# Kernel tuning notes

Measured on AMD Instinct MI355X. Metric: run time of the kernel, lower is better.

The kernel has to match this reference:

```python
import jax, jax.numpy as jnp
import numpy as np

N, E, D_IN, D_E, H, OUT, L = 16384, 131072, 128, 64, 256, 16, 4
EPS_MSG = 1e-7   # GENConv message epsilon
EPS_SM = 1e-16   # PyG softmax denominator epsilon


def _ln(x, g, b, eps=1e-5):
    mu = x.mean(-1, keepdims=True)
    var = x.var(-1, keepdims=True)
    return (x - mu) * jax.lax.rsqrt(var + eps) * g + b


def _genconv(x, src, dst, e, w1, b1, lng, lnb, w2, b2, t):
    # message: relu(x_j + edge_attr) + eps  -> [E, H]
    msg = jax.nn.relu(x[src] + e) + EPS_MSG
    # learnable-temperature segment softmax over incoming edges, per feature
    m = msg * t
    mx = jax.ops.segment_max(m, dst, num_segments=N)
    mx = jnp.where(jnp.isfinite(mx), mx, 0.0)  # empty segments -> 0
    ex = jnp.exp(m - mx[dst])
    den = jax.ops.segment_sum(ex, dst, num_segments=N)
    alpha = ex / (den[dst] + EPS_SM)
    agg = jax.ops.segment_sum(msg * alpha, dst, num_segments=N)  # [N, H]
    # root residual then 2-layer MLP: Linear -> LayerNorm -> ReLU -> Linear
    out = agg + x
    h = jax.nn.relu(_ln(out @ w1 + b1, lng, lnb))
    return h @ w2 + b2


def setup_inputs() -> dict:
    key = jax.random.key(0)
    ks = jax.random.split(key, 10)
    gl = lambda k, shape, fan: jax.random.normal(k, shape, jnp.float32) / np.sqrt(fan).astype(np.float32)
    return {
        "x": jax.random.normal(ks[0], (N, D_IN), jnp.float32),
        "edge_index": jax.random.randint(ks[1], (2, E), 0, N, dtype=jnp.int32),
        "edge_attr": jax.random.normal(ks[2], (E, D_E), jnp.float32),
        "enc_w": gl(ks[3], (D_IN, H), D_IN), "enc_b": jnp.zeros((H,), jnp.float32),
        "ee_w": gl(ks[4], (D_E, H), D_E), "ee_b": jnp.zeros((H,), jnp.float32),
        "w1": gl(ks[5], (L, H, 2 * H), H), "b1": jnp.zeros((L, 2 * H), jnp.float32),
        "lng": jnp.ones((L, 2 * H), jnp.float32), "lnb": jnp.zeros((L, 2 * H), jnp.float32),
        "w2": gl(ks[6], (L, 2 * H, H), 2 * H), "b2": jnp.zeros((L, H), jnp.float32),
        "t": jnp.ones((L,), jnp.float32),
        "ng": jnp.ones((L, H), jnp.float32), "nb": jnp.zeros((L, H), jnp.float32),
        "lin_w": gl(ks[7], (H, OUT), H), "lin_b": jnp.zeros((OUT,), jnp.float32),
    }


def reference(x, edge_index, edge_attr, enc_w, enc_b, ee_w, ee_b,
              w1, b1, lng, lnb, w2, b2, t, ng, nb, lin_w, lin_b):
    src, dst = edge_index[0], edge_index[1]
    h = x @ enc_w + enc_b                      # node encoder
    e = edge_attr @ ee_w + ee_b                # edge encoder
    # first layer: conv only (per source forward)
    h = _genconv(h, src, dst, e, w1[0], b1[0], lng[0], lnb[0], w2[0], b2[0], t[0])
    # remaining layers: res+ block = x + conv(relu(norm(x)))  (dropout off in eval)
    for i in range(1, L):
        z = jax.nn.relu(_ln(h, ng[i], nb[i]))
        h = h + _genconv(z, src, dst, e, w1[i], b1[i], lng[i], lnb[i], w2[i], b2[i], t[i])
    h = jax.nn.relu(_ln(h, ng[0], nb[0]))      # layers[0].act(layers[0].norm(x))
    return h @ lin_w + lin_b
```

## Files before the change

kernel.cpp:

```cpp
#include <hip/hip_runtime.h>
#include <stdint.h>
#include <math.h>


typedef __bf16 bf16x8 __attribute__((ext_vector_type(8)));
typedef __bf16 bf16x4 __attribute__((ext_vector_type(4)));
typedef float  f32x4  __attribute__((ext_vector_type(4)));

constexpr int NN   = 16384;
constexpr int NE   = 131072;
constexpr int DIN  = 128;
constexpr int DE   = 64;
constexpr int HD   = 256;
constexpr int HD2  = 512;

__device__ __forceinline__ void gl_lds16(const __bf16* g, __bf16* l) {
  __builtin_amdgcn_global_load_lds((const __attribute__((address_space(1))) void*)g,
                                   (__attribute__((address_space(3))) void*)l, 16, 0, 0);
}

__global__ __launch_bounds__(1024) void k_scan(const int* __restrict__ deg,
                                               int* __restrict__ row_start) {
  __shared__ int part[1024];
  const int t = threadIdx.x;
  const int base = t * 16;
  int loc[16];
  int s = 0;
  #pragma unroll
  for (int i = 0; i < 16; i++) { loc[i] = s; s += deg[base + i]; }
  part[t] = s;
  __syncthreads();
  for (int off = 1; off < 1024; off <<= 1) {
    int v = (t >= off) ? part[t - off] : 0;
    __syncthreads();
    part[t] += v;
    __syncthreads();
  }
  const int excl = (t == 0) ? 0 : part[t - 1];
  #pragma unroll
  for (int i = 0; i < 16; i++) row_start[base + i] = excl + loc[i];
}

__global__ void k_scatter(const int* __restrict__ src, const int* __restrict__ dst,
                          const int* __restrict__ row_start, int* __restrict__ cursor,
                          int2* __restrict__ csr_es) {
  int e = blockIdx.x * 256 + threadIdx.x;
  if (e >= NE) return;
  const int d = dst[e];
  const int p = atomicAdd(&cursor[d], 1);
  csr_es[row_start[d] + p] = make_int2(e, src[e]);
}

__global__ __launch_bounds__(256)
void k_sortw(const int* __restrict__ row_start, const int* __restrict__ deg,
             int2* __restrict__ csr_es, int* __restrict__ posmap) {
  const int wv   = threadIdx.x >> 6;
  const int lane = threadIdx.x & 63;
  const int node = blockIdx.x * 4 + wv;
  if (node >= NN) return;
  const int st = __builtin_amdgcn_readfirstlane(row_start[node]);
  const int dg = __builtin_amdgcn_readfirstlane(deg[node]);
  if (dg <= 1) {
    if (dg == 1 && lane == 0) posmap[csr_es[st].x] = st;
    return;
  }
  if (dg <= 64) {
    int2 pr = make_int2(0x7fffffff, 0);
    if (lane < dg) pr = csr_es[st + lane];
    int rank = 0;
    for (int j = 0; j < dg; j++) {
      const int ej = __builtin_amdgcn_readlane(pr.x, j);
      if (lane < dg && ej < pr.x) rank++;
    }
    if (lane < dg) {
      csr_es[st + rank] = pr;
      posmap[pr.x] = st + rank;
    }
  } else if (lane == 0) {
    for (int a = 1; a < dg; a++) {
      int2 k = csr_es[st + a];
      int b = a - 1;
      while (b >= 0 && csr_es[st + b].x > k.x) { csr_es[st + b + 1] = csr_es[st + b]; b--; }
      csr_es[st + b + 1] = k;
    }
    for (int a = 0; a < dg; a++) posmap[csr_es[st + a].x] = st + a;
  }
}

__global__ void k_prep(const float* __restrict__ enc_w, const float* __restrict__ ee_w,
                       const float* __restrict__ w1, const float* __restrict__ w2,
                       const int* __restrict__ dst, int* __restrict__ deg,
                       __bf16* __restrict__ enc_wT, __bf16* __restrict__ ee_wT,
                       __bf16* __restrict__ w1T, __bf16* __restrict__ w2T) {
  int i = blockIdx.x * 256 + threadIdx.x;
  const int S0 = DIN * HD, S1 = DE * HD, S2 = 4 * HD * HD2, S3 = 4 * HD2 * HD;
  if (i < S0) { int k = i / HD, n = i % HD; enc_wT[n * DIN + k] = (__bf16)enc_w[i]; return; }
  i -= S0;
  if (i < S1) { int k = i / HD, n = i % HD; ee_wT[n * DE + k] = (__bf16)ee_w[i]; return; }
  i -= S1;
  if (i < S2) {
    int l = i / (HD * HD2), r = i % (HD * HD2), k = r / HD2, n = r % HD2;
    w1T[(size_t)l * HD * HD2 + (size_t)n * HD + k] = (__bf16)w1[i]; return;
  }
  i -= S2;
  if (i < S3) {
    int l = i / (HD2 * HD), r = i % (HD2 * HD), k = r / HD, n = r % HD;
    w2T[(size_t)l * HD2 * HD + (size_t)n * HD2 + k] = (__bf16)w2[i]; return;
  }
  i -= S3;
  if (i < NE) { atomicAdd(&deg[dst[i]], 1); return; }
}

template <int RES, int OBF, int STATS, int ESCAT, int AF32>
__global__ __launch_bounds__(256, 3)
void k_gemm(const void* __restrict__ Ap, const __bf16* __restrict__ BT,
            const float* __restrict__ bias, const float* __restrict__ R,
            float* __restrict__ Cf, __bf16* __restrict__ Cb,
            const int* __restrict__ posmap, float2* __restrict__ pstats,
            int M, int Nn, int K) {
  __shared__ __attribute__((aligned(16))) char smem[49152];
  float (*sm)[129] = (float(*)[129])smem;
  float* sbias     = (float*)(smem + 16512);
  float2 (*pst4)[32] = (float2(*)[32])(smem + 17024);
  const __bf16* Ab = (const __bf16*)Ap;
  const float*  Af = (const float*)Ap;
  const int tid  = threadIdx.x;
  const int lane = tid & 63;
  const int wave = tid >> 6;
  const int ntn  = Nn >> 7;
  const int bid  = (int)blockIdx.x;
  const int bn   = (bid >> 3) % ntn;
  const int bm   = (bid & 7) + ((bid >> 3) / ntn) * 8;
  const size_t row0 = (size_t)bm * 128, col0 = (size_t)bn * 128;
  const int wr = (wave >> 1) * 64, wc = (wave & 1) * 64;
  const int ks = lane >> 4, fr = lane & 15;

  auto bufA = [&](int i) -> __bf16* { return (__bf16*)(smem + i * 8192); };
  auto bufB = [&](int i) -> __bf16* { return (__bf16*)(smem + 24576 + i * 8192); };

  f32x4 acc[4][4] = {};

  const int arow = tid >> 2;
  const int aksg = (tid & 3) ^ ((arow >> 1) & 3);

  auto stageB = [&](__bf16* lb, int k0) {
    gl_lds16(BT + (col0 + arow) * K + k0 + aksg * 8, &lb[tid * 8]);
    gl_lds16(BT + (col0 + arow + 64) * K + k0 + aksg * 8, &lb[(tid + 256) * 8]);
  };
  auto stageA = [&](__bf16* la, int k0) {
    gl_lds16(Ab + (row0 + arow) * K + k0 + aksg * 8, &la[tid * 8]);
    gl_lds16(Ab + (row0 + arow + 64) * K + k0 + aksg * 8, &la[(tid + 256) * 8]);
  };
  float4 p0, p1, q0, q1;
  auto loadAf = [&](int k0) {
    const float* a0p = &Af[(row0 + arow) * K + k0 + aksg * 8];
    const float* a1p = &Af[(row0 + arow + 64) * K + k0 + aksg * 8];
    p0 = *(const float4*)a0p; p1 = *(const float4*)(a0p + 4);
    q0 = *(const float4*)a1p; q1 = *(const float4*)(a1p + 4);
  };
  auto writeAf = [&](__bf16* la) {
    bf16x8 o0, o1;
    o0[0] = (__bf16)p0.x; o0[1] = (__bf16)p0.y; o0[2] = (__bf16)p0.z; o0[3] = (__bf16)p0.w;
    o0[4] = (__bf16)p1.x; o0[5] = (__bf16)p1.y; o0[6] = (__bf16)p1.z; o0[7] = (__bf16)p1.w;
    o1[0] = (__bf16)q0.x; o1[1] = (__bf16)q0.y; o1[2] = (__bf16)q0.z; o1[3] = (__bf16)q0.w;
    o1[4] = (__bf16)q1.x; o1[5] = (__bf16)q1.y; o1[6] = (__bf16)q1.z; o1[7] = (__bf16)q1.w;
    *(bf16x8*)&la[tid * 8] = o0;
    *(bf16x8*)&la[(tid + 256) * 8] = o1;
  };

  int slA[4], slB[4];
  #pragma unroll
  for (int m = 0; m < 4; m++) {
    const int rm = wr + m * 16 + fr;
    slA[m] = rm * 4 + (ks ^ ((rm >> 1) & 3));
    const int cn = wc + m * 16 + fr;
    slB[m] = cn * 4 + (ks ^ ((cn >> 1) & 3));
  }

  const int nk = K / 32;
  if (AF32) { loadAf(0); stageB(bufB(0), 0); writeAf(bufA(0)); }
  else      { stageA(bufA(0), 0); stageB(bufB(0), 0); }
  if (nk > 1) {
    if (AF32) { loadAf(32); stageB(bufB(1), 32); writeAf(bufA(1)); }
    else      { stageA(bufA(1), 32); stageB(bufB(1), 32); }
  }
  for (int t = 0; t < nk; t++) {
    const int rem = nk - 1 - t;
    const int nb3 = (t + 2) % 3;
    if (rem >= 2) {
      if (AF32) { loadAf((t + 2) * 32); stageB(bufB(nb3), (t + 2) * 32); }
      else      { stageA(bufA(nb3), (t + 2) * 32); stageB(bufB(nb3), (t + 2) * 32); }
    }
    if (AF32) {
      if (rem >= 2)      asm volatile("s_waitcnt vmcnt(8) lgkmcnt(0)" ::: "memory");
      else if (rem == 1) asm volatile("s_waitcnt vmcnt(2) lgkmcnt(0)" ::: "memory");
      else               asm volatile("s_waitcnt vmcnt(0) lgkmcnt(0)" ::: "memory");
    } else {
      if (rem >= 2)      asm volatile("s_waitcnt vmcnt(8)" ::: "memory");
      else if (rem == 1) asm volatile("s_waitcnt vmcnt(4)" ::: "memory");
      else               asm volatile("s_waitcnt vmcnt(0)" ::: "memory");
    }
    __builtin_amdgcn_s_barrier();
    __builtin_amdgcn_sched_barrier(0);
    const __bf16* la = bufA(t % 3);
    const __bf16* lb = bufB(t % 3);
    bf16x8 af[4], bfr[4];
    #pragma unroll
    for (int m = 0; m < 4; m++) af[m]  = *(const bf16x8*)&la[slA[m] * 8];
    #pragma unroll
    for (int n = 0; n < 4; n++) bfr[n] = *(const bf16x8*)&lb[slB[n] * 8];
    #pragma unroll
    for (int m = 0; m < 4; m++)
      #pragma unroll
      for (int n = 0; n < 4; n++)
        acc[m][n] = __builtin_amdgcn_mfma_f32_16x16x32_bf16(af[m], bfr[n], acc[m][n], 0, 0, 0);
    if (AF32 && rem >= 2) writeAf(bufA(nb3));
    __builtin_amdgcn_s_barrier();
  }
  __syncthreads();

  if (tid < 128) sbias[tid] = bias[col0 + tid];
  const int rbase = (wave >> 1) * 16 + ks * 4;
  const int rr = tid >> 3, cs = (tid & 7) * 16;
  #pragma unroll
  for (int m = 0; m < 4; m++) {
    if (m) __syncthreads();
    #pragma unroll
    for (int n = 0; n < 4; n++)
      #pragma unroll
      for (int r = 0; r < 4; r++)
        sm[rbase + r][wc + n * 16 + fr] = acc[m][n][r];
    __syncthreads();
    const size_t lrow = ((rr & 16) ? 64 : 0) + m * 16 + (rr & 15);
    const size_t grow = row0 + lrow;
    float v[16];
    #pragma unroll
    for (int j = 0; j < 16; j++) v[j] = sm[rr][cs + j] + sbias[cs + j];
    if (STATS) {
      float ssum = 0.f, ssq = 0.f;
      #pragma unroll
      for (int j = 0; j < 16; j++) { ssum += v[j]; ssq += v[j] * v[j]; }
      #pragma unroll
      for (int o = 1; o < 8; o <<= 1) {
        ssum += __shfl_xor(ssum, o);
        ssq  += __shfl_xor(ssq, o);
      }
      if ((tid & 7) == 0) pst4[m][rr].x = ssum, pst4[m][rr].y = ssq;
    }
    const size_t gbase = grow * Nn + col0 + cs;
    if (RES) {
      #pragma unroll
      for (int j = 0; j < 16; j += 4) {
        const float4 rv = *(const float4*)&R[gbase + j];
        v[j] += rv.x; v[j + 1] += rv.y; v[j + 2] += rv.z; v[j + 3] += rv.w;
      }
    }
    if (OBF == 0 || OBF == 2) {
      #pragma unroll
      for (int j = 0; j < 16; j += 4) {
        float4 o; o.x = v[j]; o.y = v[j + 1]; o.z = v[j + 2]; o.w = v[j + 3];
        *(float4*)&Cf[gbase + j] = o;
      }
    }
    if (OBF == 1 || OBF == 2) {
      const size_t crow = ESCAT ? (size_t)posmap[grow] : grow;
      const size_t cbase = crow * Nn + col0 + cs;
      bf16x8 o0, o1;
      #pragma unroll
      for (int j = 0; j < 8; j++) { o0[j] = (__bf16)v[j]; o1[j] = (__bf16)v[8 + j]; }
      *(bf16x8*)&Cb[cbase] = o0;
      *(bf16x8*)&Cb[cbase + 8] = o1;
    }
  }
  if (STATS) {
    __syncthreads();
    if (tid < 128) {
      const int lr = tid;
      const int hi = lr >> 6, m2 = (lr >> 4) & 3, rl = lr & 15;
      pstats[(row0 + lr) * ntn + bn] = pst4[m2][(hi << 4) | rl];
    }
  }
}

template <int RES, int WH>
__global__ __launch_bounds__(256, 3)
void k_gemm2f(const __bf16* __restrict__ c1b, const __bf16* __restrict__ BT,
              const float* __restrict__ bias, const float* __restrict__ R,
              const float2* __restrict__ pstats, const float* __restrict__ gamma,
              const float* __restrict__ beta, const float* __restrict__ g2,
              const float* __restrict__ b2, float* __restrict__ hout,
              __bf16* __restrict__ zout) {
  constexpr int K = HD2;
  constexpr int NC = HD;
  __shared__ __attribute__((aligned(16))) char smem[7424 + 36864];
  float* smu  = (float*)smem;
  float* sinv = (float*)(smem + 128);
  float* sg   = (float*)(smem + 256);
  float* sb   = (float*)(smem + 2304);
  float* sg2  = (float*)(smem + 4352);
  float* sb2  = (float*)(smem + 5376);
  float* sbias= (float*)(smem + 6400);
  char* arena = smem + 7424;
  auto bufA = [&](int i) -> __bf16* { return (__bf16*)(arena + i * 18432); };
  auto bufB = [&](int i) -> __bf16* { return (__bf16*)(arena + i * 18432 + 2048); };
  float (*sm)[264] = (float(*)[264])arena;

  const int tid = threadIdx.x, lane = tid & 63, wave = tid >> 6;
  const size_t row0 = (size_t)blockIdx.x * 32;
  const int wc = wave * 64;
  const int ks = lane >> 4, fr = lane & 15;

  if (tid < 32) {
    const float4* pp = (const float4*)&pstats[(row0 + tid) * 4];
    const float4 a0 = pp[0], a1 = pp[1];
    const float su = a0.x + a0.z + a1.x + a1.z;
    const float sq = a0.y + a0.w + a1.y + a1.w;
    const float mu = su * (1.f / K);
    smu[tid] = mu;
    sinv[tid] = rsqrtf(sq * (1.f / K) - mu * mu + 1e-5f);
  }
  sg[tid] = gamma[tid]; sg[tid + 256] = gamma[tid + 256];
  sb[tid] = beta[tid];  sb[tid + 256] = beta[tid + 256];
  sg2[tid] = g2[tid]; sb2[tid] = b2[tid]; sbias[tid] = bias[tid];
  __syncthreads();

  const int arow = tid >> 2;
  const int akg  = (tid & 3) ^ ((arow >> 1) & 3);
  f32x4 acc[2][4] = {};
  bf16x8 aReg;

  auto stageB = [&](__bf16* lb, int k0) {
    #pragma unroll
    for (int j = 0; j < 4; j++) {
      const int s = j * 256 + tid;
      const int scol = s >> 2;
      const int kg = (s & 3) ^ ((scol >> 1) & 3);
      gl_lds16(BT + (size_t)scol * K + k0 + kg * 8, &lb[s * 8]);
    }
  };
  auto loadA = [&](int k0) {
    if (tid < 128) aReg = *(const bf16x8*)&c1b[(row0 + arow) * K + k0 + akg * 8];
  };
  auto writeA = [&](__bf16* la, int k0) {
    if (tid < 128) {
      const int kb = k0 + akg * 8;
      const float mu = smu[arow], iv = sinv[arow];
      bf16x8 o;
      #pragma unroll
      for (int j = 0; j < 8; j++) {
        const float f = ((float)aReg[j] - mu) * iv * sg[kb + j] + sb[kb + j];
        o[j] = (__bf16)fmaxf(f, 0.f);
      }
      *(bf16x8*)&la[tid * 8] = o;
    }
  };

  int slA[2], slB[4];
  #pragma unroll
  for (int m = 0; m < 2; m++) {
    const int rm = m * 16 + fr;
    slA[m] = rm * 4 + (ks ^ ((rm >> 1) & 3));
  }
  #pragma unroll
  for (int n = 0; n < 4; n++) {
    const int cn = wc + n * 16 + fr;
    slB[n] = cn * 4 + (ks ^ ((cn >> 1) & 3));
  }

  const int nk = K / 32;
  loadA(0); stageB(bufB(0), 0); writeA(bufA(0), 0);
  for (int t = 0; t < nk; t++) {
    const bool more = (t + 1 < nk);
    const int cur = t & 1;
    if (more) { stageB(bufB(cur ^ 1), (t + 1) * 32); loadA((t + 1) * 32); }
    if (more) {
      if (wave < 2) asm volatile("s_waitcnt vmcnt(5) lgkmcnt(0)" ::: "memory");
      else          asm volatile("s_waitcnt vmcnt(4) lgkmcnt(0)" ::: "memory");
    } else {
      asm volatile("s_waitcnt vmcnt(0) lgkmcnt(0)" ::: "memory");
    }
    __builtin_amdgcn_s_barrier();
    __builtin_amdgcn_sched_barrier(0);
    const __bf16* la = bufA(cur);
    const __bf16* lb = bufB(cur);
    bf16x8 af[2], bfr[4];
    #pragma unroll
    for (int m = 0; m < 2; m++) af[m]  = *(const bf16x8*)&la[slA[m] * 8];
    #pragma unroll
    for (int n = 0; n < 4; n++) bfr[n] = *(const bf16x8*)&lb[slB[n] * 8];
    #pragma unroll
    for (int m = 0; m < 2; m++)
      #pragma unroll
      for (int n = 0; n < 4; n++)
        acc[m][n] = __builtin_amdgcn_mfma_f32_16x16x32_bf16(af[m], bfr[n], acc[m][n], 0, 0, 0);
    if (more) writeA(bufA(cur ^ 1), (t + 1) * 32);
    __builtin_amdgcn_s_barrier();
  }
  __syncthreads();

  #pragma unroll
  for (int m = 0; m < 2; m++)
    #pragma unroll
    for (int n = 0; n < 4; n++)
      #pragma unroll
      for (int r = 0; r < 4; r++)
        sm[m * 16 + ks * 4 + r][wc + n * 16 + fr] = acc[m][n][r];
  __syncthreads();
  const int rr = tid >> 3, c0 = (tid & 7) * 4;
  float v[32];
  float s = 0.f, sq = 0.f;
  #pragma unroll
  for (int j = 0; j < 8; j++) {
    const int c = c0 + j * 32;
    float x0 = sm[rr][c]     + sbias[c];
    float x1 = sm[rr][c + 1] + sbias[c + 1];
    float x2 = sm[rr][c + 2] + sbias[c + 2];
    float x3 = sm[rr][c + 3] + sbias[c + 3];
    if (RES) {
      const float4 rv = *(const float4*)&R[(row0 + rr) * NC + c];
      x0 += rv.x; x1 += rv.y; x2 += rv.z; x3 += rv.w;
    }
    v[j * 4] = x0; v[j * 4 + 1] = x1; v[j * 4 + 2] = x2; v[j * 4 + 3] = x3;
    s += x0 + x1 + x2 + x3;
    sq += x0 * x0 + x1 * x1 + x2 * x2 + x3 * x3;
  }
  #pragma unroll
  for (int o = 1; o < 8; o <<= 1) { s += __shfl_xor(s, o); sq += __shfl_xor(sq, o); }
  const float mu = s * (1.f / NC);
  const float inv = rsqrtf(sq * (1.f / NC) - mu * mu + 1e-5f);
  #pragma unroll
  for (int j = 0; j < 8; j++) {
    const int c = c0 + j * 32;
    if (WH) {
      float4 o;
      o.x = v[j * 4]; o.y = v[j * 4 + 1]; o.z = v[j * 4 + 2]; o.w = v[j * 4 + 3];
      *(float4*)&hout[(row0 + rr) * NC + c] = o;
    }
    bf16x4 z;
    z[0] = (__bf16)fmaxf((v[j * 4]     - mu) * inv * sg2[c]     + sb2[c],     0.f);
    z[1] = (__bf16)fmaxf((v[j * 4 + 1] - mu) * inv * sg2[c + 1] + sb2[c + 1], 0.f);
    z[2] = (__bf16)fmaxf((v[j * 4 + 2] - mu) * inv * sg2[c + 2] + sb2[c + 2], 0.f);
    z[3] = (__bf16)fmaxf((v[j * 4 + 3] - mu) * inv * sg2[c + 3] + sb2[c + 3], 0.f);
    *(bf16x4*)&zout[(row0 + rr) * NC + c] = z;
  }
}

__global__ __launch_bounds__(256)
void k_msg(const __bf16* __restrict__ zb, const __bf16* __restrict__ ecsr,
           const int* __restrict__ row_start, const int* __restrict__ deg,
           const int2* __restrict__ csr_es, const float* __restrict__ tvec,
           int layer, __bf16* __restrict__ a1) {
  const int wv   = __builtin_amdgcn_readfirstlane(threadIdx.x >> 6);
  const int lane = threadIdx.x & 63;
  const int node = blockIdx.x * 4 + wv;
  const int st = __builtin_amdgcn_readfirstlane(row_start[node]);
  const int dg = __builtin_amdgcn_readfirstlane(deg[node]);
  const float t = tvec[layer];
  const int f0 = lane * 4;

  int my_src = 0;
  if (lane < dg) my_src = csr_es[st + lane].y;
  const bf16x4 sv = *(const bf16x4*)&zb[(size_t)node * HD + f0];

  float den[4] = {0.f, 0.f, 0.f, 0.f}, agg[4] = {0.f, 0.f, 0.f, 0.f};
  const int dmain = dg < 64 ? dg : 64;
  int j = 0;
  for (; j + 8 <= dmain; j += 8) {
    bf16x4 zv[8], ev[8];
    #pragma unroll
    for (int u = 0; u < 8; u++) {
      const int sn = __builtin_amdgcn_readlane(my_src, j + u);
      zv[u] = *(const bf16x4*)&zb[(size_t)sn * HD + f0];
      ev[u] = *(const bf16x4*)&ecsr[(size_t)(st + j + u) * HD + f0];
    }
    #pragma unroll
    for (int u = 0; u < 8; u++)
      #pragma unroll
      for (int q = 0; q < 4; q++) {
        const float m  = fmaxf((float)zv[u][q] + (float)ev[u][q], 0.f) + 1e-7f;
        const float ex = __expf(m * t);
        den[q] += ex;
        agg[q] += m * ex;
      }
  }
  for (; j + 4 <= dmain; j += 4) {
    bf16x4 zv[4], ev[4];
    #pragma unroll
    for (int u = 0; u < 4; u++) {
      const int sn = __builtin_amdgcn_readlane(my_src, j + u);
      zv[u] = *(const bf16x4*)&zb[(size_t)sn * HD + f0];
      ev[u] = *(const bf16x4*)&ecsr[(size_t)(st + j + u) * HD + f0];
    }
    #pragma unroll
    for (int u = 0; u < 4; u++)
      #pragma unroll
      for (int q = 0; q < 4; q++) {
        const float m  = fmaxf((float)zv[u][q] + (float)ev[u][q], 0.f) + 1e-7f;
        const float ex = __expf(m * t);
        den[q] += ex;
        agg[q] += m * ex;
      }
  }
  for (; j < dmain; j++) {
    const int sn = __builtin_amdgcn_readlane(my_src, j);
    const bf16x4 zv = *(const bf16x4*)&zb[(size_t)sn * HD + f0];
    const bf16x4 ev = *(const bf16x4*)&ecsr[(size_t)(st + j) * HD + f0];
    #pragma unroll
    for (int q = 0; q < 4; q++) {
      const float m  = fmaxf((float)zv[q] + (float)ev[q], 0.f) + 1e-7f;
      const float ex = __expf(m * t);
      den[q] += ex;
      agg[q] += m * ex;
    }
  }
  for (int jj = 64; jj < dg; jj++) {
    const int2 pr = csr_es[st + jj];
    const bf16x4 zv = *(const bf16x4*)&zb[(size_t)pr.y * HD + f0];
    const bf16x4 ev = *(const bf16x4*)&ecsr[(size_t)(st + jj) * HD + f0];
    #pragma unroll
    for (int q = 0; q < 4; q++) {
      const float m  = fmaxf((float)zv[q] + (float)ev[q], 0.f) + 1e-7f;
      const float ex = __expf(m * t);
      den[q] += ex;
      agg[q] += m * ex;
    }
  }
  bf16x4 r;
  #pragma unroll
  for (int q = 0; q < 4; q++) {
    const float res = (dg > 0) ? agg[q] / (den[q] + 1e-16f) : 0.f;
    r[q] = (__bf16)(res + (float)sv[q]);
  }
  *(bf16x4*)&a1[(size_t)node * HD + f0] = r;
}

__global__ __launch_bounds__(256)
void k_head(const __bf16* __restrict__ zb, const float* __restrict__ lw,
            const float* __restrict__ lb, float* __restrict__ out) {
  __shared__ float slw[256 * 16];
  __shared__ __bf16 srow[16 * 256];
  const int t = threadIdx.x;
  const size_t row0 = (size_t)blockIdx.x * 16;
  #pragma unroll
  for (int j = 0; j < 16; j++) slw[j * 256 + t] = lw[j * 256 + t];
  #pragma unroll
  for (int j = 0; j < 2; j++) {
    const int c = j * 256 + t;
    ((bf16x8*)srow)[c] = ((const bf16x8*)(zb + row0 * 256))[c];
  }
  __syncthreads();
  const int rl = t >> 4, col = t & 15;
  float s = lb[col];
  for (int k0 = 0; k0 < 256; k0 += 8) {
    const bf16x8 zv = *(const bf16x8*)&srow[rl * 256 + k0];
    #pragma unroll
    for (int q = 0; q < 8; q++) s += (float)zv[q] * slw[(k0 + q) * 16 + col];
  }
  out[(row0 + rl) * 16 + col] = s;
}

extern "C" void kernel_launch(void* const* d_in, const int* in_sizes, int n_in,
                              void* d_out, int out_size, void* d_ws, size_t ws_size,
                              hipStream_t stream) {
  const float* x     = (const float*)d_in[0];
  const int*   ei    = (const int*)d_in[1];
  const float* ea    = (const float*)d_in[2];
  const float* enc_w = (const float*)d_in[3];
  const float* enc_b = (const float*)d_in[4];
  const float* ee_w  = (const float*)d_in[5];
  const float* ee_b  = (const float*)d_in[6];
  const float* w1    = (const float*)d_in[7];
  const float* b1    = (const float*)d_in[8];
  const float* lng   = (const float*)d_in[9];
  const float* lnb   = (const float*)d_in[10];
  const float* w2    = (const float*)d_in[11];
  const float* b2    = (const float*)d_in[12];
  const float* tvec  = (const float*)d_in[13];
  const float* ng    = (const float*)d_in[14];
  const float* nb    = (const float*)d_in[15];
  const float* lin_w = (const float*)d_in[16];
  const float* lin_b = (const float*)d_in[17];

  uint8_t* p = (uint8_t*)d_ws;
  auto alloc = [&](size_t bytes) { uint8_t* r = p; p += (bytes + 255) & ~(size_t)255; return r; };
  __bf16* e_csr  = (__bf16*)alloc((size_t)NE * HD * 2);
  float*  h      = (float*) alloc((size_t)NN * HD * 4);
  __bf16* hb     = (__bf16*)alloc((size_t)NN * HD * 2);
  __bf16* zb     = (__bf16*)alloc((size_t)NN * HD * 2);
  __bf16* a1     = (__bf16*)alloc((size_t)NN * HD * 2);
  __bf16* c1b    = (__bf16*)alloc((size_t)NN * HD2 * 2);
  float2* pstats = (float2*)alloc((size_t)NN * 4 * 8);
  __bf16* enc_wT = (__bf16*)alloc((size_t)HD * DIN * 2);
  __bf16* ee_wT  = (__bf16*)alloc((size_t)HD * DE * 2);
  __bf16* w1T    = (__bf16*)alloc((size_t)4 * HD2 * HD * 2);
  __bf16* w2T    = (__bf16*)alloc((size_t)4 * HD * HD2 * 2);
  int* deg       = (int*)alloc((size_t)NN * 4);
  int* cursor    = (int*)alloc((size_t)NN * 4);
  int* row_start = (int*)alloc((size_t)NN * 4);
  int* posmap    = (int*)alloc((size_t)NE * 4);
  int2* csr_es   = (int2*)alloc((size_t)NE * 8);

  const int* srcp = ei;
  const int* dstp = ei + NE;

  hipMemsetAsync(deg, 0, (size_t)NN * 8, stream);

  const int prep_total = DIN * HD + DE * HD + 4 * HD * HD2 + 4 * HD2 * HD + NE;
  k_prep<<<(prep_total + 255) / 256, 256, 0, stream>>>(enc_w, ee_w, w1, w2, dstp, deg,
                                                       enc_wT, ee_wT, w1T, w2T);
  k_scan<<<1, 1024, 0, stream>>>(deg, row_start);
  k_scatter<<<NE / 256, 256, 0, stream>>>(srcp, dstp, row_start, cursor, csr_es);
  k_sortw<<<NN / 4, 256, 0, stream>>>(row_start, deg, csr_es, posmap);

  k_gemm<0, 2, 0, 0, 1><<<(NN / 128) * (HD / 128), 256, 0, stream>>>(
      x, enc_wT, enc_b, nullptr, h, hb, nullptr, nullptr, NN, HD, DIN);
  k_gemm<0, 1, 0, 1, 1><<<(NE / 128) * (HD / 128), 256, 0, stream>>>(
      ea, ee_wT, ee_b, nullptr, nullptr, e_csr, posmap, nullptr, NE, HD, DE);

  for (int i = 0; i < 4; i++) {
    const __bf16* zin = (i == 0) ? hb : zb;
    k_msg<<<NN / 4, 256, 0, stream>>>(zin, e_csr, row_start, deg, csr_es, tvec, i, a1);
    k_gemm<0, 1, 1, 0, 0><<<(NN / 128) * (HD2 / 128), 256, 0, stream>>>(
        a1, w1T + (size_t)i * HD2 * HD, b1 + (size_t)i * HD2, nullptr, nullptr, c1b,
        nullptr, pstats, NN, HD2, HD);
    const int nidx = (i < 3) ? i + 1 : 0;
    const float* gg = ng + (size_t)nidx * HD;
    const float* bb = nb + (size_t)nidx * HD;
    if (i == 0)
      k_gemm2f<0, 1><<<NN / 32, 256, 0, stream>>>(
          c1b, w2T + (size_t)i * HD * HD2, b2 + (size_t)i * HD, nullptr, pstats,
          lng + (size_t)i * HD2, lnb + (size_t)i * HD2, gg, bb, h, zb);
    else if (i < 3)
      k_gemm2f<1, 1><<<NN / 32, 256, 0, stream>>>(
          c1b, w2T + (size_t)i * HD * HD2, b2 + (size_t)i * HD, h, pstats,
          lng + (size_t)i * HD2, lnb + (size_t)i * HD2, gg, bb, h, zb);
    else
      k_gemm2f<1, 0><<<NN / 32, 256, 0, stream>>>(
          c1b, w2T + (size_t)i * HD * HD2, b2 + (size_t)i * HD, h, pstats,
          lng + (size_t)i * HD2, lnb + (size_t)i * HD2, gg, bb, h, zb);
  }

  k_head<<<NN / 16, 256, 0, stream>>>(zb, lin_w, lin_b, (float*)d_out);
}
```

Before: 314.9 us.

## Fuse both MLP GEMMs and LayerNorm into one per-row-block kernel

Replaces the separate first GEMM (which wrote a bf16 [N,512] intermediate plus partial LN stats) and the second GEMM kernel with a single kernel that holds a 32-row tile of a1 in LDS. It computes the 512-wide hidden layer in registers, applies LayerNorm and ReLU on-chip, writes the result to LDS, and runs the second GEMM from there. This removes the global round trip of the 16 MB intermediate and one launch per layer. In exchange, each block re-reads the full W1 and W2 weights straight from global memory into registers without LDS staging. Register pressure also rises, so occupancy drops to 2 blocks per CU.

```diff
diff --git a/kernel.cpp b/kernel.cpp
--- a/kernel.cpp
+++ b/kernel.cpp
@@ -283,128 +283,163 @@
 }
 
 template <int RES, int WH>
-__global__ __launch_bounds__(256, 3)
-void k_gemm2f(const __bf16* __restrict__ c1b, const __bf16* __restrict__ BT,
-              const float* __restrict__ bias, const float* __restrict__ R,
-              const float2* __restrict__ pstats, const float* __restrict__ gamma,
-              const float* __restrict__ beta, const float* __restrict__ g2,
-              const float* __restrict__ b2, float* __restrict__ hout,
-              __bf16* __restrict__ zout) {
-  constexpr int K = HD2;
-  constexpr int NC = HD;
-  __shared__ __attribute__((aligned(16))) char smem[7424 + 36864];
-  float* smu  = (float*)smem;
-  float* sinv = (float*)(smem + 128);
-  float* sg   = (float*)(smem + 256);
-  float* sb   = (float*)(smem + 2304);
-  float* sg2  = (float*)(smem + 4352);
-  float* sb2  = (float*)(smem + 5376);
-  float* sbias= (float*)(smem + 6400);
-  char* arena = smem + 7424;
-  auto bufA = [&](int i) -> __bf16* { return (__bf16*)(arena + i * 18432); };
-  auto bufB = [&](int i) -> __bf16* { return (__bf16*)(arena + i * 18432 + 2048); };
-  float (*sm)[264] = (float(*)[264])arena;
+__global__ __launch_bounds__(256, 2)
+void k_mlp(const __bf16* __restrict__ a1, const __bf16* __restrict__ w1T,
+           const float* __restrict__ b1v, const float* __restrict__ g1,
+           const float* __restrict__ bln1, const __bf16* __restrict__ w2T,
+           const float* __restrict__ b2v, const float* __restrict__ R,
+           const float* __restrict__ g2, const float* __restrict__ bln2,
+           float* __restrict__ hout, __bf16* __restrict__ zout) {
+  __shared__ __attribute__((aligned(16))) char smem[60928];
+  float* sg1    = (float*)smem;
+  float* sb1    = (float*)(smem + 2048);
+  float* sbias1 = (float*)(smem + 4096);
+  float* sg2    = (float*)(smem + 6144);
+  float* sb2    = (float*)(smem + 7168);
+  float* sbias2 = (float*)(smem + 8192);
+  float2* wred  = (float2*)(smem + 9216);
+  float2* lnrow = (float2*)(smem + 10240);
+  __bf16* a1t   = (__bf16*)(smem + 10496);
+  __bf16* a2t   = (__bf16*)(smem + 26880);
+  float (*sm)[264] = (float(*)[264])(smem + 26880);
 
   const int tid = threadIdx.x, lane = tid & 63, wave = tid >> 6;
   const size_t row0 = (size_t)blockIdx.x * 32;
-  const int wc = wave * 64;
   const int ks = lane >> 4, fr = lane & 15;
 
+  sg1[tid] = g1[tid];     sg1[tid + 256] = g1[tid + 256];
+  sb1[tid] = bln1[tid];   sb1[tid + 256] = bln1[tid + 256];
+  sbias1[tid] = b1v[tid]; sbias1[tid + 256] = b1v[tid + 256];
+  sg2[tid] = g2[tid]; sb2[tid] = bln2[tid]; sbias2[tid] = b2v[tid];
+
+  #pragma unroll
+  for (int j = 0; j < 4; j++) {
+    const int s = j * 256 + tid;
+    const int r = s >> 5;
+    const int cl = (s & 31) ^ (r & 31);
+    gl_lds16(a1 + (row0 + r) * HD + cl * 8, &a1t[s * 8]);
+  }
+  __syncthreads();
+
+  f32x4 acc1[2][8] = {};
+  {
+    auto loadB1 = [&](int t, bf16x8* b) {
+      const int k0 = t * 32;
+      #pragma unroll
+      for (int n = 0; n < 8; n++) {
+        const int col = wave * 128 + n * 16 + fr;
+        b[n] = *(const bf16x8*)&w1T[(size_t)col * HD + k0 + ks * 8];
+      }
+    };
+    bf16x8 bA[8], bB[8];
+    loadB1(0, bA);
+    #pragma unroll
+    for (int t = 0; t < 8; t++) {
+      bf16x8* bc = (t & 1) ? bB : bA;
+      bf16x8* bn = (t & 1) ? bA : bB;
+      if (t + 1 < 8) loadB1(t + 1, bn);
+      bf16x8 af[2];
+      #pragma unroll
+      for (int m = 0; m < 2; m++) {
+        const int rm = m * 16 + fr;
+        af[m] = *(const bf16x8*)&a1t[(rm * 32 + ((4 * t + ks) ^ (rm & 31))) * 8];
+      }
+      #pragma unroll
+      for (int m = 0; m < 2; m++)
+        #pragma unroll
+        for (int n = 0; n < 8; n++)
+          acc1[m][n] = __builtin_amdgcn_mfma_f32_16x16x32_bf16(af[m], bc[n], acc1[m][n], 0, 0, 0);
+    }
+  }
+  #pragma unroll
+  for (int m = 0; m < 2; m++)
+    #pragma unroll
+    for (int n = 0; n < 8; n++) {
+      const int col = wave * 128 + n * 16 + fr;
+      const float bv = sbias1[col];
+      #pragma unroll
+      for (int r = 0; r < 4; r++) acc1[m][n][r] += bv;
+    }
+  #pragma unroll
+  for (int m = 0; m < 2; m++)
+    #pragma unroll
+    for (int r = 0; r < 4; r++) {
+      float s = 0.f, q = 0.f;
+      #pragma unroll
+      for (int n = 0; n < 8; n++) { const float v = acc1[m][n][r]; s += v; q += v * v; }
+      #pragma unroll
+      for (int o = 1; o < 16; o <<= 1) { s += __shfl_xor(s, o); q += __shfl_xor(q, o); }
+      if (fr == 0) {
+        const int row = m * 16 + ks * 4 + r;
+        wred[wave * 32 + row].x = s;
+        wred[wave * 32 + row].y = q;
+      }
+    }
+  __syncthreads();
   if (tid < 32) {
-    const float4* pp = (const float4*)&pstats[(row0 + tid) * 4];
-    const float4 a0 = pp[0], a1 = pp[1];
-    const float su = a0.x + a0.z + a1.x + a1.z;
-    const float sq = a0.y + a0.w + a1.y + a1.w;
-    const float mu = su * (1.f / K);
-    smu[tid] = mu;
-    sinv[tid] = rsqrtf(sq * (1.f / K) - mu * mu + 1e-5f);
-  }
-  sg[tid] = gamma[tid]; sg[tid + 256] = gamma[tid + 256];
-  sb[tid] = beta[tid];  sb[tid + 256] = beta[tid + 256];
-  sg2[tid] = g2[tid]; sb2[tid] = b2[tid]; sbias[tid] = bias[tid];
-  __syncthreads();
-
-  const int arow = tid >> 2;
-  const int akg  = (tid & 3) ^ ((arow >> 1) & 3);
-  f32x4 acc[2][4] = {};
-  bf16x8 aReg;
-
-  auto stageB = [&](__bf16* lb, int k0) {
-    #pragma unroll
-    for (int j = 0; j < 4; j++) {
-      const int s = j * 256 + tid;
-      const int scol = s >> 2;
-      const int kg = (s & 3) ^ ((scol >> 1) & 3);
-      gl_lds16(BT + (size_t)scol * K + k0 + kg * 8, &lb[s * 8]);
-    }
-  };
-  auto loadA = [&](int k0) {
-    if (tid < 128) aReg = *(const bf16x8*)&c1b[(row0 + arow) * K + k0 + akg * 8];
-  };
-  auto writeA = [&](__bf16* la, int k0) {
-    if (tid < 128) {
-      const int kb = k0 + akg * 8;
-      const float mu = smu[arow], iv = sinv[arow];
-      bf16x8 o;
-      #pragma unroll
-      for (int j = 0; j < 8; j++) {
-        const float f = ((float)aReg[j] - mu) * iv * sg[kb + j] + sb[kb + j];
-        o[j] = (__bf16)fmaxf(f, 0.f);
-      }
-      *(bf16x8*)&la[tid * 8] = o;
-    }
-  };
-
-  int slA[2], slB[4];
-  #pragma unroll
-  for (int m = 0; m < 2; m++) {
-    const int rm = m * 16 + fr;
-    slA[m] = rm * 4 + (ks ^ ((rm >> 1) & 3));
-  }
-  #pragma unroll
-  for (int n = 0; n < 4; n++) {
-    const int cn = wc + n * 16 + fr;
-    slB[n] = cn * 4 + (ks ^ ((cn >> 1) & 3));
-  }
-
-  const int nk = K / 32;
-  loadA(0); stageB(bufB(0), 0); writeA(bufA(0), 0);
-  for (int t = 0; t < nk; t++) {
-    const bool more = (t + 1 < nk);
-    const int cur = t & 1;
-    if (more) { stageB(bufB(cur ^ 1), (t + 1) * 32); loadA((t + 1) * 32); }
-    if (more) {
-      if (wave < 2) asm volatile("s_waitcnt vmcnt(5) lgkmcnt(0)" ::: "memory");
-      else          asm volatile("s_waitcnt vmcnt(4) lgkmcnt(0)" ::: "memory");
-    } else {
-      asm volatile("s_waitcnt vmcnt(0) lgkmcnt(0)" ::: "memory");
-    }
-    __builtin_amdgcn_s_barrier();
-    __builtin_amdgcn_sched_barrier(0);
-    const __bf16* la = bufA(cur);
-    const __bf16* lb = bufB(cur);
-    bf16x8 af[2], bfr[4];
-    #pragma unroll
-    for (int m = 0; m < 2; m++) af[m]  = *(const bf16x8*)&la[slA[m] * 8];
-    #pragma unroll
-    for (int n = 0; n < 4; n++) bfr[n] = *(const bf16x8*)&lb[slB[n] * 8];
-    #pragma unroll
-    for (int m = 0; m < 2; m++)
-      #pragma unroll
-      for (int n = 0; n < 4; n++)
-        acc[m][n] = __builtin_amdgcn_mfma_f32_16x16x32_bf16(af[m], bfr[n], acc[m][n], 0, 0, 0);
-    if (more) writeA(bufA(cur ^ 1), (t + 1) * 32);
-    __builtin_amdgcn_s_barrier();
-  }
-  __syncthreads();
-
+    float s = 0.f, q = 0.f;
+    #pragma unroll
+    for (int w = 0; w < 4; w++) { s += wred[w * 32 + tid].x; q += wred[w * 32 + tid].y; }
+    const float mu = s * (1.f / HD2);
+    lnrow[tid].x = mu;
+    lnrow[tid].y = rsqrtf(q * (1.f / HD2) - mu * mu + 1e-5f);
+  }
+  __syncthreads();
   #pragma unroll
   for (int m = 0; m < 2; m++)
     #pragma unroll
+    for (int r = 0; r < 4; r++) {
+      const int row = m * 16 + ks * 4 + r;
+      const float mu = lnrow[row].x, iv = lnrow[row].y;
+      #pragma unroll
+      for (int n = 0; n < 8; n++) {
+        const int col = wave * 128 + n * 16 + fr;
+        const float f = (acc1[m][n][r] - mu) * iv * sg1[col] + sb1[col];
+        const int chunk = col >> 3, sub = col & 7;
+        a2t[(row * 64 + (chunk ^ (row & 63))) * 8 + sub] = (__bf16)fmaxf(f, 0.f);
+      }
+    }
+  __syncthreads();
+
+  f32x4 acc2[2][4] = {};
+  {
+    auto loadB2 = [&](int t, bf16x8* b) {
+      const int k0 = t * 32;
+      #pragma unroll
+      for (int n = 0; n < 4; n++) {
+        const int col = wave * 64 + n * 16 + fr;
+        b[n] = *(const bf16x8*)&w2T[(size_t)col * HD2 + k0 + ks * 8];
+      }
+    };
+    bf16x8 bA[4], bB[4];
+    loadB2(0, bA);
+    #pragma unroll
+    for (int t = 0; t < 16; t++) {
+      bf16x8* bc = (t & 1) ? bB : bA;
+      bf16x8* bn = (t & 1) ? bA : bB;
+      if (t + 1 < 16) loadB2(t + 1, bn);
+      bf16x8 af[2];
+      #pragma unroll
+      for (int m = 0; m < 2; m++) {
+        const int rm = m * 16 + fr;
+        af[m] = *(const bf16x8*)&a2t[(rm * 64 + ((4 * t + ks) ^ (rm & 63))) * 8];
+      }
+      #pragma unroll
+      for (int m = 0; m < 2; m++)
+        #pragma unroll
+        for (int n = 0; n < 4; n++)
+          acc2[m][n] = __builtin_amdgcn_mfma_f32_16x16x32_bf16(af[m], bc[n], acc2[m][n], 0, 0, 0);
+    }
+  }
+  __syncthreads();
+
+  #pragma unroll
+  for (int m = 0; m < 2; m++)
+    #pragma unroll
     for (int n = 0; n < 4; n++)
       #pragma unroll
       for (int r = 0; r < 4; r++)
-        sm[m * 16 + ks * 4 + r][wc + n * 16 + fr] = acc[m][n][r];
+        sm[m * 16 + ks * 4 + r][wave * 64 + n * 16 + fr] = acc2[m][n][r];
   __syncthreads();
   const int rr = tid >> 3, c0 = (tid & 7) * 4;
   float v[32];
@@ -412,12 +447,12 @@
   #pragma unroll
   for (int j = 0; j < 8; j++) {
     const int c = c0 + j * 32;
-    float x0 = sm[rr][c]     + sbias[c];
-    float x1 = sm[rr][c + 1] + sbias[c + 1];
-    float x2 = sm[rr][c + 2] + sbias[c + 2];
-    float x3 = sm[rr][c + 3] + sbias[c + 3];
+    float x0 = sm[rr][c]     + sbias2[c];
+    float x1 = sm[rr][c + 1] + sbias2[c + 1];
+    float x2 = sm[rr][c + 2] + sbias2[c + 2];
+    float x3 = sm[rr][c + 3] + sbias2[c + 3];
     if (RES) {
-      const float4 rv = *(const float4*)&R[(row0 + rr) * NC + c];
+      const float4 rv = *(const float4*)&R[(row0 + rr) * HD + c];
       x0 += rv.x; x1 += rv.y; x2 += rv.z; x3 += rv.w;
     }
     v[j * 4] = x0; v[j * 4 + 1] = x1; v[j * 4 + 2] = x2; v[j * 4 + 3] = x3;
@@ -426,22 +461,22 @@
   }
   #pragma unroll
   for (int o = 1; o < 8; o <<= 1) { s += __shfl_xor(s, o); sq += __shfl_xor(sq, o); }
-  const float mu = s * (1.f / NC);
-  const float inv = rsqrtf(sq * (1.f / NC) - mu * mu + 1e-5f);
+  const float mu = s * (1.f / HD);
+  const float inv = rsqrtf(sq * (1.f / HD) - mu * mu + 1e-5f);
   #pragma unroll
   for (int j = 0; j < 8; j++) {
     const int c = c0 + j * 32;
     if (WH) {
       float4 o;
       o.x = v[j * 4]; o.y = v[j * 4 + 1]; o.z = v[j * 4 + 2]; o.w = v[j * 4 + 3];
-      *(float4*)&hout[(row0 + rr) * NC + c] = o;
+      *(float4*)&hout[(row0 + rr) * HD + c] = o;
     }
     bf16x4 z;
     z[0] = (__bf16)fmaxf((v[j * 4]     - mu) * inv * sg2[c]     + sb2[c],     0.f);
     z[1] = (__bf16)fmaxf((v[j * 4 + 1] - mu) * inv * sg2[c + 1] + sb2[c + 1], 0.f);
     z[2] = (__bf16)fmaxf((v[j * 4 + 2] - mu) * inv * sg2[c + 2] + sb2[c + 2], 0.f);
     z[3] = (__bf16)fmaxf((v[j * 4 + 3] - mu) * inv * sg2[c + 3] + sb2[c + 3], 0.f);
-    *(bf16x4*)&zout[(row0 + rr) * NC + c] = z;
+    *(bf16x4*)&zout[(row0 + rr) * HD + c] = z;
   }
 }
 
@@ -588,8 +623,6 @@
   __bf16* hb     = (__bf16*)alloc((size_t)NN * HD * 2);
   __bf16* zb     = (__bf16*)alloc((size_t)NN * HD * 2);
   __bf16* a1     = (__bf16*)alloc((size_t)NN * HD * 2);
-  __bf16* c1b    = (__bf16*)alloc((size_t)NN * HD2 * 2);
-  float2* pstats = (float2*)alloc((size_t)NN * 4 * 8);
   __bf16* enc_wT = (__bf16*)alloc((size_t)HD * DIN * 2);
   __bf16* ee_wT  = (__bf16*)alloc((size_t)HD * DE * 2);
   __bf16* w1T    = (__bf16*)alloc((size_t)4 * HD2 * HD * 2);
@@ -620,24 +653,27 @@
   for (int i = 0; i < 4; i++) {
     const __bf16* zin = (i == 0) ? hb : zb;
     k_msg<<<NN / 4, 256, 0, stream>>>(zin, e_csr, row_start, deg, csr_es, tvec, i, a1);
-    k_gemm<0, 1, 1, 0, 0><<<(NN / 128) * (HD2 / 128), 256, 0, stream>>>(
-        a1, w1T + (size_t)i * HD2 * HD, b1 + (size_t)i * HD2, nullptr, nullptr, c1b,
-        nullptr, pstats, NN, HD2, HD);
     const int nidx = (i < 3) ? i + 1 : 0;
     const float* gg = ng + (size_t)nidx * HD;
     const float* bb = nb + (size_t)nidx * HD;
     if (i == 0)
-      k_gemm2f<0, 1><<<NN / 32, 256, 0, stream>>>(
-          c1b, w2T + (size_t)i * HD * HD2, b2 + (size_t)i * HD, nullptr, pstats,
-          lng + (size_t)i * HD2, lnb + (size_t)i * HD2, gg, bb, h, zb);
+      k_mlp<0, 1><<<NN / 32, 256, 0, stream>>>(
+          a1, w1T + (size_t)i * HD2 * HD, b1 + (size_t)i * HD2,
+          lng + (size_t)i * HD2, lnb + (size_t)i * HD2,
+          w2T + (size_t)i * HD * HD2, b2 + (size_t)i * HD,
+          nullptr, gg, bb, h, zb);
     else if (i < 3)
-      k_gemm2f<1, 1><<<NN / 32, 256, 0, stream>>>(
-          c1b, w2T + (size_t)i * HD * HD2, b2 + (size_t)i * HD, h, pstats,
-          lng + (size_t)i * HD2, lnb + (size_t)i * HD2, gg, bb, h, zb);
+      k_mlp<1, 1><<<NN / 32, 256, 0, stream>>>(
+          a1, w1T + (size_t)i * HD2 * HD, b1 + (size_t)i * HD2,
+          lng + (size_t)i * HD2, lnb + (size_t)i * HD2,
+          w2T + (size_t)i * HD * HD2, b2 + (size_t)i * HD,
+          h, gg, bb, h, zb);
     else
-      k_gemm2f<1, 0><<<NN / 32, 256, 0, stream>>>(
-          c1b, w2T + (size_t)i * HD * HD2, b2 + (size_t)i * HD, h, pstats,
-          lng + (size_t)i * HD2, lnb + (size_t)i * HD2, gg, bb, h, zb);
+      k_mlp<1, 0><<<NN / 32, 256, 0, stream>>>(
+          a1, w1T + (size_t)i * HD2 * HD, b1 + (size_t)i * HD2,
+          lng + (size_t)i * HD2, lnb + (size_t)i * HD2,
+          w2T + (size_t)i * HD * HD2, b2 + (size_t)i * HD,
+          h, gg, bb, h, zb);
   }
 
   k_head<<<NN / 16, 256, 0, stream>>>(zb, lin_w, lin_b, (float*)d_out);
```

New measurement: 324.3 us. +3.0%, slower.
